# Optimization experiments

Measured on AMD Instinct MI355X. Metric: run time of the kernel, lower is better.

The kernel has to match this reference:

```python
import jax, jax.numpy as jnp
import numpy as np

N = 50000      # nodes
E = 800000     # edges (before self loops)
IN = 256       # in_channels
HID = 64       # hidden_channels
HEADS = 2
NEG_SLOPE = 0.2
BN_EPS = 1e-5


def setup_inputs() -> dict:
    key = jax.random.key(0)
    ks = jax.random.split(key, 16)
    def g(i, shape, scale=0.05):
        return jax.random.normal(ks[i], shape, dtype=jnp.float32) * scale
    return {
        "x": jax.random.normal(ks[0], (N, IN), dtype=jnp.float32),
        "edge_index": jax.random.randint(ks[1], (2, E), 0, N, dtype=jnp.int64).astype(jnp.int32),
        # conv1 (GATv2, heads=2, concat)
        "W1l": g(2, (IN, HEADS * HID)), "b1l": jnp.zeros(HEADS * HID, jnp.float32),
        "W1r": g(3, (IN, HEADS * HID)), "b1r": jnp.zeros(HEADS * HID, jnp.float32),
        "att1": g(4, (HEADS, HID)), "bias1": jnp.zeros(HEADS * HID, jnp.float32),
        "bn1_g": jnp.ones(HEADS * HID, jnp.float32), "bn1_b": jnp.zeros(HEADS * HID, jnp.float32),
        "bn1_m": jnp.zeros(HEADS * HID, jnp.float32), "bn1_v": jnp.ones(HEADS * HID, jnp.float32),
        # conv2 (GATv2, heads=1)
        "W2l": g(5, (HEADS * HID, HID)), "b2l": jnp.zeros(HID, jnp.float32),
        "W2r": g(6, (HEADS * HID, HID)), "b2r": jnp.zeros(HID, jnp.float32),
        "att2": g(7, (1, HID)), "bias2": jnp.zeros(HID, jnp.float32),
        "bn2_g": jnp.ones(HID, jnp.float32), "bn2_b": jnp.zeros(HID, jnp.float32),
        "bn2_m": jnp.zeros(HID, jnp.float32), "bn2_v": jnp.ones(HID, jnp.float32),
        # classifier
        "Wc": g(8, (HID, 1)), "bc": jnp.zeros(1, jnp.float32),
    }


def _gatv2(x, src, dst, Wl, bl, Wr, br, att, bias, heads, ch, n):
    # GATv2: e_ij = att . leaky_relu(Wl x_j + Wr x_i); segment softmax over dst; out_i = sum alpha_ij Wl x_j
    xl = (x @ Wl + bl).reshape(n, heads, ch)  # source transform [N,H,C]
    xr = (x @ Wr + br).reshape(n, heads, ch)  # target transform [N,H,C]
    e = jax.nn.leaky_relu(xl[src] + xr[dst], NEG_SLOPE)        # [E,H,C]
    logits = jnp.einsum('ehc,hc->eh', e, att)                  # [E,H]
    m = jax.ops.segment_max(logits, dst, num_segments=n)       # [N,H]
    p = jnp.exp(logits - m[dst])
    s = jax.ops.segment_sum(p, dst, num_segments=n)            # [N,H]
    alpha = p / s[dst]                                         # [E,H]
    out = jax.ops.segment_sum(alpha[:, :, None] * xl[src], dst, num_segments=n)  # [N,H,C]
    return out.reshape(n, heads * ch) + bias


def _bn(x, g, b, m, v):
    return (x - m) * jax.lax.rsqrt(v + BN_EPS) * g + b


def reference(x, edge_index, W1l, b1l, W1r, b1r, att1, bias1,
              bn1_g, bn1_b, bn1_m, bn1_v,
              W2l, b2l, W2r, b2r, att2, bias2,
              bn2_g, bn2_b, bn2_m, bn2_v, Wc, bc):
    n = x.shape[0]
    loop = jnp.arange(n, dtype=edge_index.dtype)  # add_self_loops=True
    src = jnp.concatenate([edge_index[0], loop])
    dst = jnp.concatenate([edge_index[1], loop])
    h = _gatv2(x, src, dst, W1l, b1l, W1r, b1r, att1, bias1, HEADS, HID, n)
    h = jax.nn.elu(_bn(h, bn1_g, bn1_b, bn1_m, bn1_v))
    h = _gatv2(h, src, dst, W2l, b2l, W2r, b2r, att2, bias2, 1, HID, n)
    h = jax.nn.elu(_bn(h, bn2_g, bn2_b, bn2_m, bn2_v))
    return jax.nn.sigmoid(h @ Wc + bc)
```

## Files before the change

### kernel.cpp

```cpp
#include <hip/hip_runtime.h>
#include <hip/hip_bf16.h>
#include <cstddef>

#define NN 50000
#define EE 800000
#define TE 850000
#define INC 256
#define C1 128
#define C2 64
#define NCHUNK 49

typedef unsigned short ushort_t;
typedef short bf16x8 __attribute__((ext_vector_type(8)));
typedef float f32x4 __attribute__((ext_vector_type(4)));

__device__ inline ushort_t bf16r(float f) {
    unsigned u = __float_as_uint(f);
    unsigned r = (u + 0x7fffu + ((u >> 16) & 1u)) >> 16;
    return (ushort_t)r;
}
#define BF2F(u) (__uint_as_float(((unsigned)(u)) << 16))
#define LOF(u) (__uint_as_float((u) << 16))
#define HIF(u) (__uint_as_float((u) & 0xffff0000u))


__global__ void k_zero(int* p, int n) {
    int i = blockIdx.x * blockDim.x + threadIdx.x;
    if (i < n) p[i] = 0;
}

__global__ void k_count(const int* __restrict__ ei, int* __restrict__ deg,
                        int* __restrict__ rank) {
    int e = blockIdx.x * blockDim.x + threadIdx.x;
    if (e >= TE) return;
    int dst = (e < EE) ? ei[EE + e] : (e - EE);
    rank[e] = atomicAdd(&deg[dst], 1);
}

__global__ void k_scan1(const int* __restrict__ deg, int* __restrict__ incl,
                        int* __restrict__ totals) {
    __shared__ int lds[1024];
    int t = threadIdx.x;
    int i = blockIdx.x * 1024 + t;
    int v = (i < NN) ? deg[i] : 0;
    lds[t] = v;
    __syncthreads();
    for (int off = 1; off < 1024; off <<= 1) {
        int add = (t >= off) ? lds[t - off] : 0;
        __syncthreads();
        lds[t] += add;
        __syncthreads();
    }
    if (i < NN) incl[i] = lds[t];
    if (t == 1023) totals[blockIdx.x] = lds[t];
}

__global__ void k_scan2(const int* __restrict__ totals, int* __restrict__ chunkoff) {
    int t = threadIdx.x;
    int orig = (t < NCHUNK) ? totals[t] : 0;
    int v = orig;
    for (int off = 1; off < 64; off <<= 1) {
        int u = __shfl_up(v, off, 64);
        if (t >= off) v += u;
    }
    if (t < NCHUNK) chunkoff[t] = v - orig;
}

__global__ void k_scan3(const int* __restrict__ incl, const int* __restrict__ deg,
                        const int* __restrict__ chunkoff, int* __restrict__ rowstart) {
    int i = blockIdx.x * blockDim.x + threadIdx.x;
    if (i == 0) rowstart[NN] = TE;
    if (i >= NN) return;
    rowstart[i] = incl[i] - deg[i] + chunkoff[i >> 10];
}

__global__ void k_scatter(const int* __restrict__ ei, const int* __restrict__ rank,
                          const int* __restrict__ rowstart, int* __restrict__ ssrc) {
    int e = blockIdx.x * blockDim.x + threadIdx.x;
    if (e >= TE) return;
    int s, d;
    if (e < EE) { s = ei[e]; d = ei[EE + e]; }
    else        { s = e - EE; d = s; }
    ssrc[rowstart[d] + rank[e]] = s;
}

__global__ void k_filldst(const int* __restrict__ rowstart, int* __restrict__ sdst) {
    int i = blockIdx.x * blockDim.x + threadIdx.x;
    if (i >= NN) return;
    int rs = rowstart[i], re = rowstart[i + 1];
    for (int j = rs; j < re; j++) sdst[j] = i;
}


__global__ void k_cast4(const float* __restrict__ src, ushort_t* __restrict__ dst, int n4) {
    int i = blockIdx.x * blockDim.x + threadIdx.x;
    if (i >= n4) return;
    float4 a = ((const float4*)src)[i];
    ushort4 o;
    o.x = bf16r(a.x); o.y = bf16r(a.y); o.z = bf16r(a.z); o.w = bf16r(a.w);
    ((ushort4*)dst)[i] = o;
}

__global__ void k_prep_w(const float* __restrict__ Wl, const float* __restrict__ Wr,
                         const float* __restrict__ bl, const float* __restrict__ br,
                         ushort_t* __restrict__ Wt, float* __restrict__ biasf,
                         int K, int HALF) {
    int n = blockIdx.x;
    int k = threadIdx.x;
    const float* W = (n < HALF) ? Wl : Wr;
    int c = (n < HALF) ? n : n - HALF;
    Wt[(size_t)n * K + k] = bf16r(W[(size_t)k * HALF + c]);
    if (n == 0 && k < 2 * HALF) biasf[k] = (k < HALF) ? bl[k] : br[k - HALF];
}


template <int K, int NCOL>
__global__ __launch_bounds__(256) void k_gemm_mfma(const ushort_t* __restrict__ A,
                                                   const ushort_t* __restrict__ Bt,
                                                   const float* __restrict__ bias,
                                                   ushort_t* __restrict__ C, int M) {
    __shared__ __align__(16) ushort_t As[128 * 40];
    __shared__ __align__(16) ushort_t Bs[128 * 40];
    int tid = threadIdx.x;
    int bm = blockIdx.x * 128;
    int bn = blockIdx.y * 128;
    int w = tid >> 6, l = tid & 63;
    int wm = (w & 1) * 64, wn = (w >> 1) * 64;
    int lm = l & 15, half = l >> 4;

    f32x4 zero = {0.f, 0.f, 0.f, 0.f};
    f32x4 acc[4][4];
#pragma unroll
    for (int a = 0; a < 4; a++)
#pragma unroll
        for (int b = 0; b < 4; b++) acc[a][b] = zero;

    for (int k0 = 0; k0 < K; k0 += 32) {
#pragma unroll
        for (int q = 0; q < 2; q++) {
            int seg = q * 256 + tid;
            int m = seg >> 2;
            int ko = (seg & 3) * 8;
            *(float4*)&As[m * 40 + ko] = *(const float4*)&A[(size_t)(bm + m) * K + k0 + ko];
            *(float4*)&Bs[m * 40 + ko] = *(const float4*)&Bt[(size_t)(bn + m) * K + k0 + ko];
        }
        __syncthreads();
        bf16x8 af[4], bfr[4];
#pragma unroll
        for (int mi = 0; mi < 4; mi++)
            af[mi] = *(const bf16x8*)&As[(wm + mi * 16 + lm) * 40 + half * 8];
#pragma unroll
        for (int ni = 0; ni < 4; ni++)
            bfr[ni] = *(const bf16x8*)&Bs[(wn + ni * 16 + lm) * 40 + half * 8];
#pragma unroll
        for (int mi = 0; mi < 4; mi++)
#pragma unroll
            for (int ni = 0; ni < 4; ni++)
                acc[mi][ni] = __builtin_amdgcn_mfma_f32_16x16x32_bf16(
                    af[mi], bfr[ni], acc[mi][ni], 0, 0, 0);
        __syncthreads();
    }
#pragma unroll
    for (int ni = 0; ni < 4; ni++) {
        int col = bn + wn + ni * 16 + lm;
        float bv = bias[col];
#pragma unroll
        for (int mi = 0; mi < 4; mi++) {
            int rbase = bm + wm + mi * 16 + half * 4;
#pragma unroll
            for (int r = 0; r < 4; r++) {
                int row = rbase + r;
                if (row < M) C[(size_t)row * NCOL + col] = bf16r(acc[mi][ni][r] + bv);
            }
        }
    }
}


__device__ inline float lrelu_dot2(unsigned ua, unsigned ub, float at_lo, float at_hi) {
    float alo = __uint_as_float(ua << 16), ahi = __uint_as_float(ua & 0xffff0000u);
    float blo = __uint_as_float(ub << 16), bhi = __uint_as_float(ub & 0xffff0000u);
    float t0 = alo + blo, t1 = ahi + bhi;
    float l0 = fmaxf(t0, 0.f) + 0.2f * fminf(t0, 0.f);
    float l1 = fmaxf(t1, 0.f) + 0.2f * fminf(t1, 0.f);
    return at_lo * l0 + at_hi * l1;
}

template <int STRIDE, int ITS, int HEADS>
__global__ __launch_bounds__(256) void k_edge(
    const ushort_t* __restrict__ xlr,
    const int* __restrict__ ssrc, const int* __restrict__ sdst,
    const float* __restrict__ att, float* __restrict__ spk) {
    int l = threadIdx.x & 63;
    int wv = threadIdx.x >> 6;
    int q = l & 3;
    int j = blockIdx.x * 64 + wv * 16 + (l >> 2);
    if (j >= TE) return;
    int src = ssrc[j], dst = sdst[j];
    const ushort_t* xl = xlr + (size_t)src * STRIDE;
    const ushort_t* xr = xlr + (size_t)dst * STRIDE + STRIDE / 2;
    float w[HEADS];
#pragma unroll
    for (int h = 0; h < HEADS; h++) w[h] = 0.f;
#pragma unroll
    for (int it = 0; it < ITS; it++) {
        int c = q + 4 * it;
        uint4 a = *(const uint4*)&xl[c * 8];
        uint4 b = *(const uint4*)&xr[c * 8];
        float4 t0 = *(const float4*)&att[c * 8];
        float4 t1 = *(const float4*)&att[c * 8 + 4];
        int h = (HEADS == 2 && it >= ITS / 2) ? 1 : 0;
        float d = lrelu_dot2(a.x, b.x, t0.x, t0.y)
                + lrelu_dot2(a.y, b.y, t0.z, t0.w)
                + lrelu_dot2(a.z, b.z, t1.x, t1.y)
                + lrelu_dot2(a.w, b.w, t1.z, t1.w);
        w[h] += d;
    }
#pragma unroll
    for (int h = 0; h < HEADS; h++) {
        w[h] += __shfl_xor(w[h], 1, 64);
        w[h] += __shfl_xor(w[h], 2, 64);
    }
    if (q == 0) {
        if (HEADS == 2) {
            ((float4*)spk)[j] = make_float4(__int_as_float(src), __expf(w[0]), __expf(w[1]), 0.f);
        } else {
            ((float2*)spk)[j] = make_float2(__int_as_float(src), __expf(w[0]));
        }
    }
}


__global__ __launch_bounds__(256) void k_aggr1(
    const ushort_t* __restrict__ xlr, const float* __restrict__ spk,
    const int* __restrict__ rowstart,
    const float* __restrict__ bias,
    const float* __restrict__ g, const float* __restrict__ b,
    const float* __restrict__ m, const float* __restrict__ v,
    ushort_t* __restrict__ out) {
    int lane = threadIdx.x & 63;
    int i = blockIdx.x * 4 + (threadIdx.x >> 6);
    if (i >= NN) return;
    int head = lane >> 5;
    int row = rowstart[i], end = rowstart[i + 1];
    float ax = 0.f, ay = 0.f, s = 0.f;
    int j = row;
    for (; j + 8 <= end; j += 8) {
        float4 e[8];
        unsigned u[8];
#pragma unroll
        for (int k = 0; k < 8; k++) e[k] = ((const float4*)spk)[j + k];
#pragma unroll
        for (int k = 0; k < 8; k++)
            u[k] = *(const unsigned*)&xlr[(size_t)__float_as_int(e[k].x) * 256 + 2 * lane];
#pragma unroll
        for (int k = 0; k < 8; k++) {
            float p = head ? e[k].z : e[k].y;
            ax += p * LOF(u[k]);
            ay += p * HIF(u[k]);
            s += p;
        }
    }
    if (j + 4 <= end) {
        float4 e[4];
        unsigned u[4];
#pragma unroll
        for (int k = 0; k < 4; k++) e[k] = ((const float4*)spk)[j + k];
#pragma unroll
        for (int k = 0; k < 4; k++)
            u[k] = *(const unsigned*)&xlr[(size_t)__float_as_int(e[k].x) * 256 + 2 * lane];
#pragma unroll
        for (int k = 0; k < 4; k++) {
            float p = head ? e[k].z : e[k].y;
            ax += p * LOF(u[k]);
            ay += p * HIF(u[k]);
            s += p;
        }
        j += 4;
    }
    for (; j < end; j++) {
        float4 e0 = ((const float4*)spk)[j];
        float p = head ? e0.z : e0.y;
        unsigned u = *(const unsigned*)&xlr[(size_t)__float_as_int(e0.x) * 256 + 2 * lane];
        ax += p * LOF(u);
        ay += p * HIF(u);
        s += p;
    }
    float inv = 1.f / s;
    float2 bb = ((const float2*)bias)[lane];
    float2 mm = ((const float2*)m)[lane];
    float2 vv = ((const float2*)v)[lane];
    float2 gg = ((const float2*)g)[lane];
    float2 bb2 = ((const float2*)b)[lane];
    float ox = ax * inv + bb.x, oy = ay * inv + bb.y;
    ox = (ox - mm.x) * rsqrtf(vv.x + 1e-5f) * gg.x + bb2.x;
    oy = (oy - mm.y) * rsqrtf(vv.y + 1e-5f) * gg.y + bb2.y;
    ox = (ox > 0.f) ? ox : (__expf(ox) - 1.f);
    oy = (oy > 0.f) ? oy : (__expf(oy) - 1.f);
    unsigned wpack = (unsigned)bf16r(ox) | ((unsigned)bf16r(oy) << 16);
    *(unsigned*)&out[(size_t)i * C1 + 2 * lane] = wpack;
}

__global__ __launch_bounds__(256) void k_aggr2(
    const ushort_t* __restrict__ xlr, const float* __restrict__ spk,
    const int* __restrict__ rowstart,
    const float* __restrict__ bias,
    const float* __restrict__ g, const float* __restrict__ b,
    const float* __restrict__ m, const float* __restrict__ v,
    const float* __restrict__ Wc, const float* __restrict__ bc,
    float* __restrict__ out) {
    int lane = threadIdx.x & 63;
    int c2 = lane & 31;
    int i = blockIdx.x * 8 + (threadIdx.x >> 6) * 2 + (lane >> 5);
    if (i >= NN) return;
    int row = rowstart[i], end = rowstart[i + 1];
    float ax = 0.f, ay = 0.f, s = 0.f;
    int j = row;
    for (; j + 4 <= end; j += 4) {
        float2 e[4];
        unsigned u[4];
#pragma unroll
        for (int k = 0; k < 4; k++) e[k] = ((const float2*)spk)[j + k];
#pragma unroll
        for (int k = 0; k < 4; k++)
            u[k] = *(const unsigned*)&xlr[(size_t)__float_as_int(e[k].x) * 128 + 2 * c2];
#pragma unroll
        for (int k = 0; k < 4; k++) {
            ax += e[k].y * LOF(u[k]);
            ay += e[k].y * HIF(u[k]);
            s += e[k].y;
        }
    }
    for (; j < end; j++) {
        float2 e0 = ((const float2*)spk)[j];
        unsigned u = *(const unsigned*)&xlr[(size_t)__float_as_int(e0.x) * 128 + 2 * c2];
        ax += e0.y * LOF(u);
        ay += e0.y * HIF(u);
        s += e0.y;
    }
    float inv = 1.f / s;
    float2 bb = ((const float2*)bias)[c2];
    float2 mm = ((const float2*)m)[c2];
    float2 vv = ((const float2*)v)[c2];
    float2 gg = ((const float2*)g)[c2];
    float2 bb2 = ((const float2*)b)[c2];
    float ox = ax * inv + bb.x, oy = ay * inv + bb.y;
    ox = (ox - mm.x) * rsqrtf(vv.x + 1e-5f) * gg.x + bb2.x;
    oy = (oy - mm.y) * rsqrtf(vv.y + 1e-5f) * gg.y + bb2.y;
    ox = (ox > 0.f) ? ox : (__expf(ox) - 1.f);
    oy = (oy > 0.f) ? oy : (__expf(oy) - 1.f);
    float2 wc = ((const float2*)Wc)[c2];
    float z = ox * wc.x + oy * wc.y;
    z += __shfl_xor(z, 16, 64);
    z += __shfl_xor(z, 8, 64);
    z += __shfl_xor(z, 4, 64);
    z += __shfl_xor(z, 2, 64);
    z += __shfl_xor(z, 1, 64);
    if (c2 == 0) out[i] = 1.f / (1.f + __expf(-(z + bc[0])));
}


extern "C" void kernel_launch(void* const* d_in, const int* in_sizes, int n_in,
                              void* d_out, int out_size, void* d_ws, size_t ws_size,
                              hipStream_t stream) {
    const float* x    = (const float*)d_in[0];
    const int*   ei   = (const int*)d_in[1];
    const float* W1l  = (const float*)d_in[2];
    const float* b1l  = (const float*)d_in[3];
    const float* W1r  = (const float*)d_in[4];
    const float* b1r  = (const float*)d_in[5];
    const float* att1 = (const float*)d_in[6];
    const float* bias1= (const float*)d_in[7];
    const float* bn1g = (const float*)d_in[8];
    const float* bn1b = (const float*)d_in[9];
    const float* bn1m = (const float*)d_in[10];
    const float* bn1v = (const float*)d_in[11];
    const float* W2l  = (const float*)d_in[12];
    const float* b2l  = (const float*)d_in[13];
    const float* W2r  = (const float*)d_in[14];
    const float* b2r  = (const float*)d_in[15];
    const float* att2 = (const float*)d_in[16];
    const float* bias2= (const float*)d_in[17];
    const float* bn2g = (const float*)d_in[18];
    const float* bn2b = (const float*)d_in[19];
    const float* bn2m = (const float*)d_in[20];
    const float* bn2v = (const float*)d_in[21];
    const float* Wc   = (const float*)d_in[22];
    const float* bc   = (const float*)d_in[23];
    float* out = (float*)d_out;

    char* ws = (char*)d_ws;
    size_t off = 0;
    auto alloc = [&](size_t bytes) {
        size_t o = off;
        off += (bytes + 255) & ~(size_t)255;
        return o;
    };
    ushort_t* xb    = (ushort_t*)(ws + alloc((size_t)(NN + 128) * 256 * 2));
    ushort_t* xlr1  = (ushort_t*)(ws + alloc((size_t)NN * 256 * 2));
    ushort_t* h1b   = (ushort_t*)(ws + alloc((size_t)(NN + 128) * 128 * 2));
    ushort_t* Wt1   = (ushort_t*)(ws + alloc((size_t)256 * 256 * 2));
    float*    biasf1= (float*)(ws + alloc(256 * 4));
    ushort_t* Wt2   = (ushort_t*)(ws + alloc((size_t)128 * 128 * 2));
    float*    biasf2= (float*)(ws + alloc(128 * 4));
    int* deg      = (int*)(ws + alloc((size_t)NN * 4));
    int* incl     = (int*)(ws + alloc((size_t)NN * 4));
    int* rowstart = (int*)(ws + alloc((size_t)(NN + 1) * 4));
    int* totals   = (int*)(ws + alloc(64 * 4));
    int* chunkoff = (int*)(ws + alloc(64 * 4));
    int* rank     = (int*)(ws + alloc((size_t)TE * 4));
    int* ssrc     = (int*)(ws + alloc((size_t)TE * 4));
    int* sdst     = (int*)(ws + alloc((size_t)TE * 4));
    float* spk1 = (float*)xb;
    float* spk2 = spk1;
    ushort_t* xlr2 = xlr1;

    k_zero<<<(NN + 255) / 256, 256, 0, stream>>>(deg, NN);
    k_count<<<(TE + 255) / 256, 256, 0, stream>>>(ei, deg, rank);
    k_scan1<<<NCHUNK, 1024, 0, stream>>>(deg, incl, totals);
    k_scan2<<<1, 64, 0, stream>>>(totals, chunkoff);
    k_scan3<<<(NN + 255) / 256, 256, 0, stream>>>(incl, deg, chunkoff, rowstart);
    k_scatter<<<(TE + 255) / 256, 256, 0, stream>>>(ei, rank, rowstart, ssrc);
    k_filldst<<<(NN + 255) / 256, 256, 0, stream>>>(rowstart, sdst);

    int n4x = NN * INC / 4;
    k_cast4<<<(n4x + 255) / 256, 256, 0, stream>>>(x, xb, n4x);
    k_prep_w<<<256, 256, 0, stream>>>(W1l, W1r, b1l, b1r, Wt1, biasf1, 256, 128);
    k_prep_w<<<128, 128, 0, stream>>>(W2l, W2r, b2l, b2r, Wt2, biasf2, 128, 64);

    int eb = (TE + 63) / 64;

    dim3 gg1((NN + 127) / 128, 2);
    k_gemm_mfma<256, 256><<<gg1, 256, 0, stream>>>(xb, Wt1, biasf1, xlr1, NN);
    k_edge<256, 4, 2><<<eb, 256, 0, stream>>>(xlr1, ssrc, sdst, att1, spk1);
    k_aggr1<<<(NN + 3) / 4, 256, 0, stream>>>(xlr1, spk1, rowstart, bias1,
                                              bn1g, bn1b, bn1m, bn1v, h1b);

    dim3 gg2((NN + 127) / 128, 1);
    k_gemm_mfma<128, 128><<<gg2, 256, 0, stream>>>(h1b, Wt2, biasf2, xlr2, NN);
    k_edge<128, 2, 1><<<eb, 256, 0, stream>>>(xlr2, ssrc, sdst, att2, spk2);
    k_aggr2<<<(NN + 7) / 8, 256, 0, stream>>>(xlr2, spk2, rowstart, bias2,
                                              bn2g, bn2b, bn2m, bn2v, Wc, bc, out);
}
```

Measured before the change: 356.0 us.

## Fuse GATv2 edge-score computation into per-node aggregation kernels

Removes the separate per-edge score kernels and the intermediate spk buffer. Attention logits are now computed inside the CSR aggregation kernels: one wavefront handles a destination node, splits its edges across sub-waves, and reduces the logits with shuffles. The sdst array and the k_filldst kernel are dropped, which saves the launches and the write and re-read of per-edge scores. In exchange there is more shuffle work per edge, and the softmax still skips max subtraction, as the old code already did.

```diff
diff --git a/kernel.cpp b/kernel.cpp
--- a/kernel.cpp
+++ b/kernel.cpp
@@ -19,9 +19,10 @@
     unsigned r = (u + 0x7fffu + ((u >> 16) & 1u)) >> 16;
     return (ushort_t)r;
 }
-#define BF2F(u) (__uint_as_float(((unsigned)(u)) << 16))
 #define LOF(u) (__uint_as_float((u) << 16))
 #define HIF(u) (__uint_as_float((u) & 0xffff0000u))
+#define LRELU(t) (fmaxf((t), 0.f) + 0.2f * fminf((t), 0.f))
+#define ELU(t) ((t) > 0.f ? (t) : (__expf(t) - 1.f))
 
 
 __global__ void k_zero(int* p, int n) {
@@ -84,13 +85,6 @@
     ssrc[rowstart[d] + rank[e]] = s;
 }
 
-__global__ void k_filldst(const int* __restrict__ rowstart, int* __restrict__ sdst) {
-    int i = blockIdx.x * blockDim.x + threadIdx.x;
-    if (i >= NN) return;
-    int rs = rowstart[i], re = rowstart[i + 1];
-    for (int j = rs; j < re; j++) sdst[j] = i;
-}
-
 
 __global__ void k_cast4(const float* __restrict__ src, ushort_t* __restrict__ dst, int n4) {
     int i = blockIdx.x * blockDim.x + threadIdx.x;
@@ -177,63 +171,9 @@
 }
 
 
-__device__ inline float lrelu_dot2(unsigned ua, unsigned ub, float at_lo, float at_hi) {
-    float alo = __uint_as_float(ua << 16), ahi = __uint_as_float(ua & 0xffff0000u);
-    float blo = __uint_as_float(ub << 16), bhi = __uint_as_float(ub & 0xffff0000u);
-    float t0 = alo + blo, t1 = ahi + bhi;
-    float l0 = fmaxf(t0, 0.f) + 0.2f * fminf(t0, 0.f);
-    float l1 = fmaxf(t1, 0.f) + 0.2f * fminf(t1, 0.f);
-    return at_lo * l0 + at_hi * l1;
-}
-
-template <int STRIDE, int ITS, int HEADS>
-__global__ __launch_bounds__(256) void k_edge(
-    const ushort_t* __restrict__ xlr,
-    const int* __restrict__ ssrc, const int* __restrict__ sdst,
-    const float* __restrict__ att, float* __restrict__ spk) {
-    int l = threadIdx.x & 63;
-    int wv = threadIdx.x >> 6;
-    int q = l & 3;
-    int j = blockIdx.x * 64 + wv * 16 + (l >> 2);
-    if (j >= TE) return;
-    int src = ssrc[j], dst = sdst[j];
-    const ushort_t* xl = xlr + (size_t)src * STRIDE;
-    const ushort_t* xr = xlr + (size_t)dst * STRIDE + STRIDE / 2;
-    float w[HEADS];
-#pragma unroll
-    for (int h = 0; h < HEADS; h++) w[h] = 0.f;
-#pragma unroll
-    for (int it = 0; it < ITS; it++) {
-        int c = q + 4 * it;
-        uint4 a = *(const uint4*)&xl[c * 8];
-        uint4 b = *(const uint4*)&xr[c * 8];
-        float4 t0 = *(const float4*)&att[c * 8];
-        float4 t1 = *(const float4*)&att[c * 8 + 4];
-        int h = (HEADS == 2 && it >= ITS / 2) ? 1 : 0;
-        float d = lrelu_dot2(a.x, b.x, t0.x, t0.y)
-                + lrelu_dot2(a.y, b.y, t0.z, t0.w)
-                + lrelu_dot2(a.z, b.z, t1.x, t1.y)
-                + lrelu_dot2(a.w, b.w, t1.z, t1.w);
-        w[h] += d;
-    }
-#pragma unroll
-    for (int h = 0; h < HEADS; h++) {
-        w[h] += __shfl_xor(w[h], 1, 64);
-        w[h] += __shfl_xor(w[h], 2, 64);
-    }
-    if (q == 0) {
-        if (HEADS == 2) {
-            ((float4*)spk)[j] = make_float4(__int_as_float(src), __expf(w[0]), __expf(w[1]), 0.f);
-        } else {
-            ((float2*)spk)[j] = make_float2(__int_as_float(src), __expf(w[0]));
-        }
-    }
-}
-
-
-__global__ __launch_bounds__(256) void k_aggr1(
-    const ushort_t* __restrict__ xlr, const float* __restrict__ spk,
-    const int* __restrict__ rowstart,
+__global__ __launch_bounds__(256) void k_fused1(
+    const ushort_t* __restrict__ xlr, const int* __restrict__ rowstart,
+    const int* __restrict__ ssrc, const float* __restrict__ att,
     const float* __restrict__ bias,
     const float* __restrict__ g, const float* __restrict__ b,
     const float* __restrict__ m, const float* __restrict__ v,
@@ -241,122 +181,183 @@
     int lane = threadIdx.x & 63;
     int i = blockIdx.x * 4 + (threadIdx.x >> 6);
     if (i >= NN) return;
-    int head = lane >> 5;
+    int hw = lane >> 5;
+    int c2 = lane & 31;
+    uint2 xru = *(const uint2*)&xlr[(size_t)i * 256 + 128 + 4 * c2];
+    float xr0 = LOF(xru.x), xr1 = HIF(xru.x), xr2 = LOF(xru.y), xr3 = HIF(xru.y);
+    float4 at = *(const float4*)&att[4 * c2];
     int row = rowstart[i], end = rowstart[i + 1];
-    float ax = 0.f, ay = 0.f, s = 0.f;
+    float a0 = 0.f, a1 = 0.f, a2 = 0.f, a3 = 0.f, s = 0.f;
     int j = row;
     for (; j + 8 <= end; j += 8) {
-        float4 e[8];
-        unsigned u[8];
-#pragma unroll
-        for (int k = 0; k < 8; k++) e[k] = ((const float4*)spk)[j + k];
-#pragma unroll
-        for (int k = 0; k < 8; k++)
-            u[k] = *(const unsigned*)&xlr[(size_t)__float_as_int(e[k].x) * 256 + 2 * lane];
-#pragma unroll
-        for (int k = 0; k < 8; k++) {
-            float p = head ? e[k].z : e[k].y;
-            ax += p * LOF(u[k]);
-            ay += p * HIF(u[k]);
+        int src[4];
+        uint2 u[4];
+#pragma unroll
+        for (int k = 0; k < 4; k++) src[k] = ssrc[j + 2 * k + hw];
+#pragma unroll
+        for (int k = 0; k < 4; k++)
+            u[k] = *(const uint2*)&xlr[(size_t)src[k] * 256 + 4 * c2];
+        float d[4], f0[4], f1[4], f2[4], f3[4];
+#pragma unroll
+        for (int k = 0; k < 4; k++) {
+            f0[k] = LOF(u[k].x); f1[k] = HIF(u[k].x);
+            f2[k] = LOF(u[k].y); f3[k] = HIF(u[k].y);
+            float t0 = f0[k] + xr0, t1 = f1[k] + xr1;
+            float t2 = f2[k] + xr2, t3 = f3[k] + xr3;
+            d[k] = at.x * LRELU(t0) + at.y * LRELU(t1)
+                 + at.z * LRELU(t2) + at.w * LRELU(t3);
+        }
+#pragma unroll
+        for (int o = 1; o <= 8; o <<= 1) {
+#pragma unroll
+            for (int k = 0; k < 4; k++) d[k] += __shfl_xor(d[k], o, 64);
+        }
+#pragma unroll
+        for (int k = 0; k < 4; k++) {
+            float p = __expf(d[k]);
+            a0 += p * f0[k]; a1 += p * f1[k];
+            a2 += p * f2[k]; a3 += p * f3[k];
             s += p;
         }
     }
-    if (j + 4 <= end) {
-        float4 e[4];
-        unsigned u[4];
-#pragma unroll
-        for (int k = 0; k < 4; k++) e[k] = ((const float4*)spk)[j + k];
-#pragma unroll
-        for (int k = 0; k < 4; k++)
-            u[k] = *(const unsigned*)&xlr[(size_t)__float_as_int(e[k].x) * 256 + 2 * lane];
-#pragma unroll
-        for (int k = 0; k < 4; k++) {
-            float p = head ? e[k].z : e[k].y;
-            ax += p * LOF(u[k]);
-            ay += p * HIF(u[k]);
-            s += p;
-        }
-        j += 4;
-    }
-    for (; j < end; j++) {
-        float4 e0 = ((const float4*)spk)[j];
-        float p = head ? e0.z : e0.y;
-        unsigned u = *(const unsigned*)&xlr[(size_t)__float_as_int(e0.x) * 256 + 2 * lane];
-        ax += p * LOF(u);
-        ay += p * HIF(u);
+    for (; j < end; j += 2) {
+        int je = j + hw;
+        bool valid = je < end;
+        int src = valid ? ssrc[je] : i;
+        uint2 uu = *(const uint2*)&xlr[(size_t)src * 256 + 4 * c2];
+        float f0 = LOF(uu.x), f1 = HIF(uu.x), f2 = LOF(uu.y), f3 = HIF(uu.y);
+        float t0 = f0 + xr0, t1 = f1 + xr1, t2 = f2 + xr2, t3 = f3 + xr3;
+        float d = at.x * LRELU(t0) + at.y * LRELU(t1)
+                + at.z * LRELU(t2) + at.w * LRELU(t3);
+        d += __shfl_xor(d, 1, 64);
+        d += __shfl_xor(d, 2, 64);
+        d += __shfl_xor(d, 4, 64);
+        d += __shfl_xor(d, 8, 64);
+        float p = valid ? __expf(d) : 0.f;
+        a0 += p * f0; a1 += p * f1; a2 += p * f2; a3 += p * f3;
         s += p;
     }
-    float inv = 1.f / s;
-    float2 bb = ((const float2*)bias)[lane];
-    float2 mm = ((const float2*)m)[lane];
-    float2 vv = ((const float2*)v)[lane];
-    float2 gg = ((const float2*)g)[lane];
-    float2 bb2 = ((const float2*)b)[lane];
-    float ox = ax * inv + bb.x, oy = ay * inv + bb.y;
-    ox = (ox - mm.x) * rsqrtf(vv.x + 1e-5f) * gg.x + bb2.x;
-    oy = (oy - mm.y) * rsqrtf(vv.y + 1e-5f) * gg.y + bb2.y;
-    ox = (ox > 0.f) ? ox : (__expf(ox) - 1.f);
-    oy = (oy > 0.f) ? oy : (__expf(oy) - 1.f);
-    unsigned wpack = (unsigned)bf16r(ox) | ((unsigned)bf16r(oy) << 16);
-    *(unsigned*)&out[(size_t)i * C1 + 2 * lane] = wpack;
-}
-
-__global__ __launch_bounds__(256) void k_aggr2(
-    const ushort_t* __restrict__ xlr, const float* __restrict__ spk,
-    const int* __restrict__ rowstart,
+    a0 += __shfl_xor(a0, 32, 64);
+    a1 += __shfl_xor(a1, 32, 64);
+    a2 += __shfl_xor(a2, 32, 64);
+    a3 += __shfl_xor(a3, 32, 64);
+    s  += __shfl_xor(s, 32, 64);
+    if (hw == 0) {
+        float inv = 1.f / s;
+        float4 bb = *(const float4*)&bias[4 * c2];
+        float4 mm = *(const float4*)&m[4 * c2];
+        float4 vv = *(const float4*)&v[4 * c2];
+        float4 gg = *(const float4*)&g[4 * c2];
+        float4 b2 = *(const float4*)&b[4 * c2];
+        float o0 = a0 * inv + bb.x, o1 = a1 * inv + bb.y;
+        float o2 = a2 * inv + bb.z, o3 = a3 * inv + bb.w;
+        o0 = (o0 - mm.x) * rsqrtf(vv.x + 1e-5f) * gg.x + b2.x;
+        o1 = (o1 - mm.y) * rsqrtf(vv.y + 1e-5f) * gg.y + b2.y;
+        o2 = (o2 - mm.z) * rsqrtf(vv.z + 1e-5f) * gg.z + b2.z;
+        o3 = (o3 - mm.w) * rsqrtf(vv.w + 1e-5f) * gg.w + b2.w;
+        o0 = ELU(o0); o1 = ELU(o1); o2 = ELU(o2); o3 = ELU(o3);
+        uint2 wp;
+        wp.x = (unsigned)bf16r(o0) | ((unsigned)bf16r(o1) << 16);
+        wp.y = (unsigned)bf16r(o2) | ((unsigned)bf16r(o3) << 16);
+        *(uint2*)&out[(size_t)i * C1 + 4 * c2] = wp;
+    }
+}
+
+__global__ __launch_bounds__(256) void k_fused2(
+    const ushort_t* __restrict__ xlr, const int* __restrict__ rowstart,
+    const int* __restrict__ ssrc, const float* __restrict__ att,
     const float* __restrict__ bias,
     const float* __restrict__ g, const float* __restrict__ b,
     const float* __restrict__ m, const float* __restrict__ v,
     const float* __restrict__ Wc, const float* __restrict__ bc,
     float* __restrict__ out) {
     int lane = threadIdx.x & 63;
-    int c2 = lane & 31;
-    int i = blockIdx.x * 8 + (threadIdx.x >> 6) * 2 + (lane >> 5);
+    int i = blockIdx.x * 4 + (threadIdx.x >> 6);
     if (i >= NN) return;
+    int qw = lane >> 4;
+    int c4 = lane & 15;
+    uint2 xru = *(const uint2*)&xlr[(size_t)i * 128 + 64 + 4 * c4];
+    float xr0 = LOF(xru.x), xr1 = HIF(xru.x), xr2 = LOF(xru.y), xr3 = HIF(xru.y);
+    float4 at = *(const float4*)&att[4 * c4];
     int row = rowstart[i], end = rowstart[i + 1];
-    float ax = 0.f, ay = 0.f, s = 0.f;
+    float a0 = 0.f, a1 = 0.f, a2 = 0.f, a3 = 0.f, s = 0.f;
     int j = row;
-    for (; j + 4 <= end; j += 4) {
-        float2 e[4];
-        unsigned u[4];
-#pragma unroll
-        for (int k = 0; k < 4; k++) e[k] = ((const float2*)spk)[j + k];
-#pragma unroll
-        for (int k = 0; k < 4; k++)
-            u[k] = *(const unsigned*)&xlr[(size_t)__float_as_int(e[k].x) * 128 + 2 * c2];
-#pragma unroll
-        for (int k = 0; k < 4; k++) {
-            ax += e[k].y * LOF(u[k]);
-            ay += e[k].y * HIF(u[k]);
-            s += e[k].y;
-        }
-    }
-    for (; j < end; j++) {
-        float2 e0 = ((const float2*)spk)[j];
-        unsigned u = *(const unsigned*)&xlr[(size_t)__float_as_int(e0.x) * 128 + 2 * c2];
-        ax += e0.y * LOF(u);
-        ay += e0.y * HIF(u);
-        s += e0.y;
+    for (; j + 8 <= end; j += 8) {
+        int src[2];
+        uint2 u[2];
+#pragma unroll
+        for (int k = 0; k < 2; k++) src[k] = ssrc[j + 4 * k + qw];
+#pragma unroll
+        for (int k = 0; k < 2; k++)
+            u[k] = *(const uint2*)&xlr[(size_t)src[k] * 128 + 4 * c4];
+        float d[2], f0[2], f1[2], f2[2], f3[2];
+#pragma unroll
+        for (int k = 0; k < 2; k++) {
+            f0[k] = LOF(u[k].x); f1[k] = HIF(u[k].x);
+            f2[k] = LOF(u[k].y); f3[k] = HIF(u[k].y);
+            float t0 = f0[k] + xr0, t1 = f1[k] + xr1;
+            float t2 = f2[k] + xr2, t3 = f3[k] + xr3;
+            d[k] = at.x * LRELU(t0) + at.y * LRELU(t1)
+                 + at.z * LRELU(t2) + at.w * LRELU(t3);
+        }
+#pragma unroll
+        for (int o = 1; o <= 8; o <<= 1) {
+#pragma unroll
+            for (int k = 0; k < 2; k++) d[k] += __shfl_xor(d[k], o, 64);
+        }
+#pragma unroll
+        for (int k = 0; k < 2; k++) {
+            float p = __expf(d[k]);
+            a0 += p * f0[k]; a1 += p * f1[k];
+            a2 += p * f2[k]; a3 += p * f3[k];
+            s += p;
+        }
+    }
+    for (; j < end; j += 4) {
+        int je = j + qw;
+        bool valid = je < end;
+        int src = valid ? ssrc[je] : i;
+        uint2 uu = *(const uint2*)&xlr[(size_t)src * 128 + 4 * c4];
+        float f0 = LOF(uu.x), f1 = HIF(uu.x), f2 = LOF(uu.y), f3 = HIF(uu.y);
+        float t0 = f0 + xr0, t1 = f1 + xr1, t2 = f2 + xr2, t3 = f3 + xr3;
+        float d = at.x * LRELU(t0) + at.y * LRELU(t1)
+                + at.z * LRELU(t2) + at.w * LRELU(t3);
+        d += __shfl_xor(d, 1, 64);
+        d += __shfl_xor(d, 2, 64);
+        d += __shfl_xor(d, 4, 64);
+        d += __shfl_xor(d, 8, 64);
+        float p = valid ? __expf(d) : 0.f;
+        a0 += p * f0; a1 += p * f1; a2 += p * f2; a3 += p * f3;
+        s += p;
+    }
+#pragma unroll
+    for (int o = 16; o <= 32; o <<= 1) {
+        a0 += __shfl_xor(a0, o, 64);
+        a1 += __shfl_xor(a1, o, 64);
+        a2 += __shfl_xor(a2, o, 64);
+        a3 += __shfl_xor(a3, o, 64);
+        s  += __shfl_xor(s, o, 64);
     }
     float inv = 1.f / s;
-    float2 bb = ((const float2*)bias)[c2];
-    float2 mm = ((const float2*)m)[c2];
-    float2 vv = ((const float2*)v)[c2];
-    float2 gg = ((const float2*)g)[c2];
-    float2 bb2 = ((const float2*)b)[c2];
-    float ox = ax * inv + bb.x, oy = ay * inv + bb.y;
-    ox = (ox - mm.x) * rsqrtf(vv.x + 1e-5f) * gg.x + bb2.x;
-    oy = (oy - mm.y) * rsqrtf(vv.y + 1e-5f) * gg.y + bb2.y;
-    ox = (ox > 0.f) ? ox : (__expf(ox) - 1.f);
-    oy = (oy > 0.f) ? oy : (__expf(oy) - 1.f);
-    float2 wc = ((const float2*)Wc)[c2];
-    float z = ox * wc.x + oy * wc.y;
-    z += __shfl_xor(z, 16, 64);
+    float4 bb = *(const float4*)&bias[4 * c4];
+    float4 mm = *(const float4*)&m[4 * c4];
+    float4 vv = *(const float4*)&v[4 * c4];
+    float4 gg = *(const float4*)&g[4 * c4];
+    float4 b2 = *(const float4*)&b[4 * c4];
+    float o0 = a0 * inv + bb.x, o1 = a1 * inv + bb.y;
+    float o2 = a2 * inv + bb.z, o3 = a3 * inv + bb.w;
+    o0 = (o0 - mm.x) * rsqrtf(vv.x + 1e-5f) * gg.x + b2.x;
+    o1 = (o1 - mm.y) * rsqrtf(vv.y + 1e-5f) * gg.y + b2.y;
+    o2 = (o2 - mm.z) * rsqrtf(vv.z + 1e-5f) * gg.z + b2.z;
+    o3 = (o3 - mm.w) * rsqrtf(vv.w + 1e-5f) * gg.w + b2.w;
+    o0 = ELU(o0); o1 = ELU(o1); o2 = ELU(o2); o3 = ELU(o3);
+    float4 wc = *(const float4*)&Wc[4 * c4];
+    float z = o0 * wc.x + o1 * wc.y + o2 * wc.z + o3 * wc.w;
+    z += __shfl_xor(z, 1, 64);
+    z += __shfl_xor(z, 2, 64);
+    z += __shfl_xor(z, 4, 64);
     z += __shfl_xor(z, 8, 64);
-    z += __shfl_xor(z, 4, 64);
-    z += __shfl_xor(z, 2, 64);
-    z += __shfl_xor(z, 1, 64);
-    if (c2 == 0) out[i] = 1.f / (1.f + __expf(-(z + bc[0])));
+    if (lane == 0) out[i] = 1.f / (1.f + __expf(-(z + bc[0])));
 }
 
 
@@ -410,9 +411,6 @@
     int* chunkoff = (int*)(ws + alloc(64 * 4));
     int* rank     = (int*)(ws + alloc((size_t)TE * 4));
     int* ssrc     = (int*)(ws + alloc((size_t)TE * 4));
-    int* sdst     = (int*)(ws + alloc((size_t)TE * 4));
-    float* spk1 = (float*)xb;
-    float* spk2 = spk1;
     ushort_t* xlr2 = xlr1;
 
     k_zero<<<(NN + 255) / 256, 256, 0, stream>>>(deg, NN);
@@ -421,24 +419,19 @@
     k_scan2<<<1, 64, 0, stream>>>(totals, chunkoff);
     k_scan3<<<(NN + 255) / 256, 256, 0, stream>>>(incl, deg, chunkoff, rowstart);
     k_scatter<<<(TE + 255) / 256, 256, 0, stream>>>(ei, rank, rowstart, ssrc);
-    k_filldst<<<(NN + 255) / 256, 256, 0, stream>>>(rowstart, sdst);
 
     int n4x = NN * INC / 4;
     k_cast4<<<(n4x + 255) / 256, 256, 0, stream>>>(x, xb, n4x);
     k_prep_w<<<256, 256, 0, stream>>>(W1l, W1r, b1l, b1r, Wt1, biasf1, 256, 128);
     k_prep_w<<<128, 128, 0, stream>>>(W2l, W2r, b2l, b2r, Wt2, biasf2, 128, 64);
 
-    int eb = (TE + 63) / 64;
-
     dim3 gg1((NN + 127) / 128, 2);
     k_gemm_mfma<256, 256><<<gg1, 256, 0, stream>>>(xb, Wt1, biasf1, xlr1, NN);
-    k_edge<256, 4, 2><<<eb, 256, 0, stream>>>(xlr1, ssrc, sdst, att1, spk1);
-    k_aggr1<<<(NN + 3) / 4, 256, 0, stream>>>(xlr1, spk1, rowstart, bias1,
-                                              bn1g, bn1b, bn1m, bn1v, h1b);
+    k_fused1<<<(NN + 3) / 4, 256, 0, stream>>>(xlr1, rowstart, ssrc, att1, bias1,
+                                               bn1g, bn1b, bn1m, bn1v, h1b);
 
     dim3 gg2((NN + 127) / 128, 1);
     k_gemm_mfma<128, 128><<<gg2, 256, 0, stream>>>(h1b, Wt2, biasf2, xlr2, NN);
-    k_edge<128, 2, 1><<<eb, 256, 0, stream>>>(xlr2, ssrc, sdst, att2, spk2);
-    k_aggr2<<<(NN + 7) / 8, 256, 0, stream>>>(xlr2, spk2, rowstart, bias2,
-                                              bn2g, bn2b, bn2m, bn2v, Wc, bc, out);
-}
+    k_fused2<<<(NN + 3) / 4, 256, 0, stream>>>(xlr2, rowstart, ssrc, att2, bias2,
+                                               bn2g, bn2b, bn2m, bn2v, Wc, bc, out);
+}
```

New measurement: 322.4 us. -9.4%, faster.
